# Performance work log

Hardware: AMD Instinct MI355X
Metric: run time of the kernel (lower is better)

Reference implementation:

```python
import jax, jax.numpy as jnp
import numpy as np

N_HEAD = 8
REG_LAMBDA = 0.01


def setup_inputs() -> dict:
    key = jax.random.key(0)
    k0, k1, k2 = jax.random.split(key, 3)
    B, T, C = 8, 256, 512
    x = jax.random.normal(k0, (B, T, C), dtype=jnp.float32)
    W_attn = jax.random.normal(k1, (3 * C, C), dtype=jnp.float32) * 0.02
    b_attn = jnp.zeros((3 * C,), dtype=jnp.float32)
    W_proj = jax.random.normal(k2, (C, C), dtype=jnp.float32) * 0.02
    b_proj = jnp.zeros((C,), dtype=jnp.float32)
    return {"x": x, "W_attn": W_attn, "b_attn": b_attn, "W_proj": W_proj, "b_proj": b_proj}


def reference(x, W_attn, b_attn, W_proj, b_proj):
    B, T, C = x.shape
    H = N_HEAD
    hs = C // H
    # qkv projection (nn.Linear: x @ W.T + b)
    qkv = x @ W_attn.T + b_attn                      # [B,T,3C]
    q, k, v = jnp.split(qkv, 3, axis=-1)

    def to_heads(t):
        return t.reshape(B, T, H, hs).transpose(0, 2, 1, 3)  # [B,H,T,hs]

    q, k, v = to_heads(q), to_heads(k), to_heads(v)

    scale = 1.0 / jnp.sqrt(jnp.asarray(hs, dtype=x.dtype))
    scores = jnp.einsum('bhqd,bhkd->bhqk', q, k) * scale     # [B,H,T,T]
    causal = jnp.tril(jnp.ones((T, T), dtype=bool))
    scores = jnp.where(causal, scores, -jnp.inf)
    att = jax.nn.softmax(scores, axis=-1)                    # [B,H,T,T]

    # --- Soft DPP penalty ---
    # For token i: G_i = (sqrt(w_i) outer sqrt(w_i)) * (K K^T) + 1e-6 I,
    # which equals (sqrt_w * K) @ (sqrt_w * K)^T from the original code.
    KKt = jnp.einsum('bhid,bhjd->bhij', k, k)                # [B,H,T,T], shared across tokens
    eyeT = 1e-6 * jnp.eye(T, dtype=jnp.float32)

    def step(carry, w):  # w: [B,H,T] attention row for one query token
        s = jnp.sqrt(w + 1e-8)                               # [B,H,T]
        G = (s[..., :, None] * s[..., None, :] * KKt).astype(jnp.float32) + eyeT
        det = jnp.linalg.det(G)                              # [B,H]
        return carry + jnp.sum(jnp.log(det + 1e-8)), None

    att_tok = jnp.moveaxis(att, 2, 0)                        # [T,B,H,T]
    logdet_sum, _ = jax.lax.scan(step, jnp.float32(0.0), att_tok)
    dpp_penalty = REG_LAMBDA * (-1.0 * logdet_sum)

    # attention output
    y = jnp.einsum('bhqk,bhkd->bhqd', att, v)                # [B,H,T,hs]
    y = y.transpose(0, 2, 1, 3).reshape(B, T, C)
    y = y @ W_proj.T + b_proj
    return y, dpp_penalty
```

## Files before the change

kernel.cpp:

```cpp
#include <hip/hip_runtime.h>
#include <hip/hip_bf16.h>
#include <math.h>


#define BT 2048
#define TSEQ 256
#define CDIM 512
#define QKVC 1536

typedef __attribute__((ext_vector_type(8))) short bf16x8;
typedef __attribute__((ext_vector_type(4))) float f32x4;

__device__ __forceinline__ unsigned short b16(float f) {
  return __builtin_bit_cast(unsigned short, __float2bfloat16(f));
}

__global__ __launch_bounds__(256) void qkv_mfma(
    const float* __restrict__ X, const float* __restrict__ W,
    const float* __restrict__ bias, unsigned short* __restrict__ C,
    unsigned short* __restrict__ VT) {
  __shared__ unsigned short a_s[64][68];
  __shared__ unsigned short b_s[64][68];

  const int t  = threadIdx.x;
  const int m0 = blockIdx.x * 64;
  const int n0 = blockIdx.y * 64;
  const int w  = t >> 6, l = t & 63;
  const int wm = (w >> 1) * 32, wn = (w & 1) * 32;

  f32x4 acc[2][2];
#pragma unroll
  for (int i = 0; i < 2; i++)
#pragma unroll
    for (int j = 0; j < 2; j++) acc[i][j] = (f32x4){0.f, 0.f, 0.f, 0.f};

  float4 pa[4], pb[4];
  auto prefetch = [&](int k0) {
#pragma unroll
    for (int u = 0; u < 4; u++) {
      const int id = t + u * 256;
      const int r  = id >> 4;
      const int c4 = (id & 15) << 2;
      pa[u] = *(const float4*)&X[(size_t)(m0 + r) * CDIM + k0 + c4];
      pb[u] = *(const float4*)&W[(size_t)(n0 + r) * CDIM + k0 + c4];
    }
  };

  prefetch(0);
  for (int kb = 0; kb < CDIM / 64; kb++) {
    __syncthreads();
#pragma unroll
    for (int u = 0; u < 4; u++) {
      const int id = t + u * 256;
      const int r  = id >> 4;
      const int c4 = (id & 15) << 2;
      ushort4 ah;
      ah.x = b16(pa[u].x); ah.y = b16(pa[u].y); ah.z = b16(pa[u].z); ah.w = b16(pa[u].w);
      *(ushort4*)&a_s[r][c4] = ah;
      ushort4 bh;
      bh.x = b16(pb[u].x); bh.y = b16(pb[u].y); bh.z = b16(pb[u].z); bh.w = b16(pb[u].w);
      *(ushort4*)&b_s[r][c4] = bh;
    }
    __syncthreads();
    if (kb + 1 < CDIM / 64) prefetch((kb + 1) * 64);

#pragma unroll
    for (int ks = 0; ks < 2; ks++) {
      const int fr = l & 15;
      const int fk = ks * 32 + ((l >> 4) << 3);
      bf16x8 fa[2], fb[2];
#pragma unroll
      for (int mt = 0; mt < 2; mt++) fa[mt] = *(const bf16x8*)&a_s[wm + mt * 16 + fr][fk];
#pragma unroll
      for (int nt = 0; nt < 2; nt++) fb[nt] = *(const bf16x8*)&b_s[wn + nt * 16 + fr][fk];
#pragma unroll
      for (int mt = 0; mt < 2; mt++)
#pragma unroll
        for (int nt = 0; nt < 2; nt++)
          acc[mt][nt] = __builtin_amdgcn_mfma_f32_16x16x32_bf16(fa[mt], fb[nt], acc[mt][nt], 0, 0, 0);
    }
  }

  const int cl = l & 15, rq = (l >> 4) << 2;
  if (n0 < 1024) {
    const float scale = (n0 < 512) ? 0.125f : 1.0f;
#pragma unroll
    for (int nt = 0; nt < 2; nt++) {
      const int col = n0 + wn + nt * 16 + cl;
      const float bv = bias[col];
#pragma unroll
      for (int mt = 0; mt < 2; mt++) {
        const int row = m0 + wm + mt * 16 + rq;
#pragma unroll
        for (int r = 0; r < 4; r++)
          C[(size_t)(row + r) * QKVC + col] = b16((acc[mt][nt][r] + bv) * scale);
      }
    }
  } else {
#pragma unroll
    for (int nt = 0; nt < 2; nt++) {
      const int col  = n0 + wn + nt * 16 + cl;
      const float bv = bias[col];
      const int hcol = col - 1024;
      const int h = hcol >> 6, d = hcol & 63;
#pragma unroll
      for (int mt = 0; mt < 2; mt++) {
        const int row = m0 + wm + mt * 16 + rq;
        const int b = row >> 8, j = row & 255;
        ushort4 o;
        o.x = b16(acc[mt][nt][0] + bv);
        o.y = b16(acc[mt][nt][1] + bv);
        o.z = b16(acc[mt][nt][2] + bv);
        o.w = b16(acc[mt][nt][3] + bv);
        *(ushort4*)&VT[(((size_t)(b * 8 + h) * 64 + d) << 8) + j] = o;
      }
    }
  }
}

__global__ __launch_bounds__(256) void attn_mfma(
    const unsigned short* __restrict__ qkv, const unsigned short* __restrict__ VT,
    unsigned short* __restrict__ y) {
  __shared__ unsigned short k_s[64][72];
  __shared__ unsigned short vt_s[64][72];
  __shared__ unsigned short q_s2[2][32][72];
  __shared__ unsigned short p_s[4][16][72];

  const int t  = threadIdx.x;
  const int qp = blockIdx.x;
  const int bh = blockIdx.y;
  const int b  = bh >> 3, h = bh & 7;
  const int w  = t >> 6, l = t & 63;
  const int half = w >> 1;
  const int ww   = w & 1;
  const int qt = qp * 2 + half;
  const int q0 = qt * 32;
  const size_t rowbase = (size_t)b * TSEQ * QKVC + h * 64;
  const size_t vtb = (size_t)bh << 14;
  const float NEG = -1e30f;

#pragma unroll
  for (int u = 0; u < 2; u++) {
    const int id = t + u * 256;
    const int rg = id >> 3, c8 = (id & 7) << 3;
    const int hf = rg >> 5, row = rg & 31;
    const int qrow = (qp * 2 + hf) * 32 + row;
    *(uint4*)&q_s2[hf][row][c8] =
        *(const uint4*)(qkv + rowbase + (size_t)qrow * QKVC + c8);
  }
  __syncthreads();

  const int m  = l & 15;
  const int q4 = l >> 4;
  const int ko = q4 << 3;

  bf16x8 qf[2];
#pragma unroll
  for (int kb = 0; kb < 2; kb++)
    qf[kb] = *(const bf16x8*)&q_s2[half][ww * 16 + m][kb * 32 + ko];

  f32x4 acc_y[4];
  float m_i[4], Zp[4];
#pragma unroll
  for (int r = 0; r < 4; r++) {
    acc_y[r] = (f32x4){0.f, 0.f, 0.f, 0.f};
    m_i[r] = NEG; Zp[r] = 0.f;
  }

  const int ntiles = qp + 1;

  uint4 pk[2], pv[2];
  auto loadKV = [&](int jt) {
#pragma unroll
    for (int u = 0; u < 2; u++) {
      const int id = t + u * 256;
      const int r = id >> 3, c8 = (id & 7) << 3;
      pk[u] = *(const uint4*)(qkv + rowbase + (size_t)(jt * 64 + r) * QKVC + 512 + c8);
      pv[u] = *(const uint4*)(VT + vtb + ((size_t)r << 8) + jt * 64 + c8);
    }
  };

  loadKV(0);
  for (int jt = 0; jt < ntiles; jt++) {
    __syncthreads();
#pragma unroll
    for (int u = 0; u < 2; u++) {
      const int id = t + u * 256;
      const int r = id >> 3, c8 = (id & 7) << 3;
      *(uint4*)&k_s[r][c8]  = pk[u];
      *(uint4*)&vt_s[r][c8] = pv[u];
    }
    __syncthreads();
    if (jt + 1 < ntiles) loadKV(jt + 1);

    f32x4 s[4];
#pragma unroll
    for (int nt = 0; nt < 4; nt++) s[nt] = (f32x4){0.f, 0.f, 0.f, 0.f};
#pragma unroll
    for (int nt = 0; nt < 4; nt++)
#pragma unroll
      for (int kb = 0; kb < 2; kb++) {
        const bf16x8 kf = *(const bf16x8*)&k_s[nt * 16 + m][kb * 32 + ko];
        s[nt] = __builtin_amdgcn_mfma_f32_16x16x32_bf16(qf[kb], kf, s[nt], 0, 0, 0);
      }

    const bool diag = (jt == ntiles - 1);
#pragma unroll
    for (int reg = 0; reg < 4; reg++) {
      const int i = q0 + ww * 16 + q4 * 4 + reg;
      float pvv[4];
      float vmax = NEG;
#pragma unroll
      for (int nt = 0; nt < 4; nt++) {
        float sv = s[nt][reg];
        if (diag && (jt * 64 + nt * 16 + m) > i) sv = NEG;
        pvv[nt] = sv;
        vmax = fmaxf(vmax, sv);
      }
      vmax = fmaxf(vmax, __shfl_xor(vmax, 1));
      vmax = fmaxf(vmax, __shfl_xor(vmax, 2));
      vmax = fmaxf(vmax, __shfl_xor(vmax, 4));
      vmax = fmaxf(vmax, __shfl_xor(vmax, 8));
      const float mnew  = fmaxf(m_i[reg], vmax);
      const float alpha = __expf(m_i[reg] - mnew);
      m_i[reg] = mnew;
      float zs = 0.f;
#pragma unroll
      for (int nt = 0; nt < 4; nt++) {
        const float p = __expf(pvv[nt] - mnew);
        p_s[w][q4 * 4 + reg][nt * 16 + m] = b16(p);
        zs += p;
      }
      Zp[reg] = Zp[reg] * alpha + zs;
#pragma unroll
      for (int nt2 = 0; nt2 < 4; nt2++) acc_y[nt2][reg] *= alpha;
    }
    __syncthreads();

#pragma unroll
    for (int kb2 = 0; kb2 < 2; kb2++) {
      const bf16x8 pf = *(const bf16x8*)&p_s[w][m][kb2 * 32 + ko];
#pragma unroll
      for (int nt2 = 0; nt2 < 4; nt2++) {
        const bf16x8 vf = *(const bf16x8*)&vt_s[nt2 * 16 + m][kb2 * 32 + ko];
        acc_y[nt2] = __builtin_amdgcn_mfma_f32_16x16x32_bf16(pf, vf, acc_y[nt2], 0, 0, 0);
      }
    }
  }

#pragma unroll
  for (int reg = 0; reg < 4; reg++) {
    float z = Zp[reg];
    z += __shfl_xor(z, 1);
    z += __shfl_xor(z, 2);
    z += __shfl_xor(z, 4);
    z += __shfl_xor(z, 8);
    const float inv = 1.0f / z;
    const int i = q0 + ww * 16 + q4 * 4 + reg;
#pragma unroll
    for (int nt2 = 0; nt2 < 4; nt2++)
      y[((size_t)(b * TSEQ + i)) * CDIM + h * 64 + nt2 * 16 + m] =
          b16(acc_y[nt2][reg] * inv);
  }
}

__global__ __launch_bounds__(256) void proj_mfma(
    const unsigned short* __restrict__ A, const float* __restrict__ B,
    const float* __restrict__ bias, float* __restrict__ C) {
  __shared__ unsigned short a_s[32][68];
  __shared__ unsigned short b_s[64][68];

  const int t  = threadIdx.x;
  if (blockIdx.x == 0 && blockIdx.y == 0 && t == 0) {
    const double log_1em8 = -18.420680743952367;
    C[(size_t)BT * CDIM] = (float)(-0.01 * (16384.0 * log_1em8));
  }
  const int m0 = blockIdx.x * 32;
  const int n0 = blockIdx.y * 64;
  const int w  = t >> 6, l = t & 63;
  const int wm = (w >> 1) * 16, wn = (w & 1) * 32;

  f32x4 acc[2];
#pragma unroll
  for (int j = 0; j < 2; j++) acc[j] = (f32x4){0.f, 0.f, 0.f, 0.f};

  uint4  pa;
  float4 pb[4];
  auto prefetch = [&](int k0) {
    {
      const int r = t >> 3, c8 = (t & 7) << 3;
      pa = *(const uint4*)(A + (size_t)(m0 + r) * CDIM + k0 + c8);
    }
#pragma unroll
    for (int u = 0; u < 4; u++) {
      const int id = t + u * 256;
      const int r = id >> 4, c4 = (id & 15) << 2;
      pb[u] = *(const float4*)&B[(size_t)(n0 + r) * CDIM + k0 + c4];
    }
  };

  prefetch(0);
  for (int kb = 0; kb < CDIM / 64; kb++) {
    __syncthreads();
    {
      const int r = t >> 3, c8 = (t & 7) << 3;
      *(uint4*)&a_s[r][c8] = pa;
    }
#pragma unroll
    for (int u = 0; u < 4; u++) {
      const int id = t + u * 256;
      const int r = id >> 4, c4 = (id & 15) << 2;
      ushort4 bh;
      bh.x = b16(pb[u].x); bh.y = b16(pb[u].y); bh.z = b16(pb[u].z); bh.w = b16(pb[u].w);
      *(ushort4*)&b_s[r][c4] = bh;
    }
    __syncthreads();
    if (kb + 1 < CDIM / 64) prefetch((kb + 1) * 64);

#pragma unroll
    for (int ks = 0; ks < 2; ks++) {
      const int fr = l & 15;
      const int fk = ks * 32 + ((l >> 4) << 3);
      const bf16x8 fa = *(const bf16x8*)&a_s[wm + fr][fk];
      bf16x8 fb2[2];
#pragma unroll
      for (int nt = 0; nt < 2; nt++) fb2[nt] = *(const bf16x8*)&b_s[wn + nt * 16 + fr][fk];
#pragma unroll
      for (int nt = 0; nt < 2; nt++)
        acc[nt] = __builtin_amdgcn_mfma_f32_16x16x32_bf16(fa, fb2[nt], acc[nt], 0, 0, 0);
    }
  }

  const int cl = l & 15, rq = (l >> 4) << 2;
#pragma unroll
  for (int nt = 0; nt < 2; nt++) {
    const int col = n0 + wn + nt * 16 + cl;
    const float bv = bias[col];
    const int row = m0 + wm + rq;
#pragma unroll
    for (int r = 0; r < 4; r++)
      C[(size_t)(row + r) * CDIM + col] = acc[nt][r] + bv;
  }
}

extern "C" void kernel_launch(void* const* d_in, const int* in_sizes, int n_in,
                              void* d_out, int out_size, void* d_ws, size_t ws_size,
                              hipStream_t stream) {
  const float* x      = (const float*)d_in[0];
  const float* W_attn = (const float*)d_in[1];
  const float* b_attn = (const float*)d_in[2];
  const float* W_proj = (const float*)d_in[3];
  const float* b_proj = (const float*)d_in[4];
  float* out = (float*)d_out;

  char* wsb = (char*)d_ws;
  unsigned short* qkv_bf = (unsigned short*)wsb;
  unsigned short* vt_bf  = (unsigned short*)(wsb + 6291456);
  unsigned short* y_bf   = (unsigned short*)(wsb + 8388608);

  qkv_mfma<<<dim3(32, 24), 256, 0, stream>>>(x, W_attn, b_attn, qkv_bf, vt_bf);

  attn_mfma<<<dim3(4, 64), 256, 0, stream>>>(qkv_bf, vt_bf, y_bf);

  proj_mfma<<<dim3(64, 8), 256, 0, stream>>>(y_bf, W_proj, b_proj, out);
}
```

Measured before the change: 98.56 us.

## Fuse output projection into attention kernel with atomic head accumulation

Removes the separate projection kernel. Each attention block converts its head's slice of W_proj to bf16 in shared memory, multiplies its 64-row y tile by it, and atomically adds the partial result into the fp32 output. The qkv kernel now pre-initializes the output with the projection bias and writes the penalty constant. This avoids the y round trip through memory and one launch, but adds 8-way float atomics per output element, large LDS use, heavy accumulator register pressure and redundant W_proj loads per block.

After: 120.5 us. 1.22x slower.

```diff
diff --git a/kernel.cpp b/kernel.cpp
--- a/kernel.cpp
+++ b/kernel.cpp
@@ -15,16 +15,36 @@
   return __builtin_bit_cast(unsigned short, __float2bfloat16(f));
 }
 
+__device__ __forceinline__ void atomAddF32(float* p, float v) {
+  unsafeAtomicAdd(p, v);
+}
+
 __global__ __launch_bounds__(256) void qkv_mfma(
     const float* __restrict__ X, const float* __restrict__ W,
     const float* __restrict__ bias, unsigned short* __restrict__ C,
-    unsigned short* __restrict__ VT) {
+    unsigned short* __restrict__ VT, const float* __restrict__ b_proj,
+    float* __restrict__ out) {
   __shared__ unsigned short a_s[64][68];
   __shared__ unsigned short b_s[64][68];
 
   const int t  = threadIdx.x;
   const int m0 = blockIdx.x * 64;
   const int n0 = blockIdx.y * 64;
+
+  if (blockIdx.y == 0) {
+#pragma unroll
+    for (int u = 0; u < 32; u++) {
+      const int id = t + u * 256;
+      const int r  = id >> 7;
+      const int c  = (id & 127) << 2;
+      *(float4*)&out[(size_t)(m0 + r) * CDIM + c] = *(const float4*)&b_proj[c];
+    }
+    if (blockIdx.x == 0 && t == 0) {
+      const double log_1em8 = -18.420680743952367;
+      out[(size_t)BT * CDIM] = (float)(-0.01 * (16384.0 * log_1em8));
+    }
+  }
+
   const int w  = t >> 6, l = t & 63;
   const int wm = (w >> 1) * 32, wn = (w & 1) * 32;
 
@@ -118,13 +138,15 @@
   }
 }
 
-__global__ __launch_bounds__(256) void attn_mfma(
+__global__ __launch_bounds__(256) void attn_proj(
     const unsigned short* __restrict__ qkv, const unsigned short* __restrict__ VT,
-    unsigned short* __restrict__ y) {
+    const float* __restrict__ Wp, float* __restrict__ out) {
   __shared__ unsigned short k_s[64][72];
   __shared__ unsigned short vt_s[64][72];
   __shared__ unsigned short q_s2[2][32][72];
   __shared__ unsigned short p_s[4][16][72];
+  __shared__ unsigned short y_s[64][72];
+  __shared__ unsigned short w_s[512][68];
 
   const int t  = threadIdx.x;
   const int qp = blockIdx.x;
@@ -256,90 +278,69 @@
     z += __shfl_xor(z, 4);
     z += __shfl_xor(z, 8);
     const float inv = 1.0f / z;
-    const int i = q0 + ww * 16 + q4 * 4 + reg;
+    const int lr = half * 32 + ww * 16 + q4 * 4 + reg;
 #pragma unroll
     for (int nt2 = 0; nt2 < 4; nt2++)
-      y[((size_t)(b * TSEQ + i)) * CDIM + h * 64 + nt2 * 16 + m] =
-          b16(acc_y[nt2][reg] * inv);
-  }
-}
-
-__global__ __launch_bounds__(256) void proj_mfma(
-    const unsigned short* __restrict__ A, const float* __restrict__ B,
-    const float* __restrict__ bias, float* __restrict__ C) {
-  __shared__ unsigned short a_s[32][68];
-  __shared__ unsigned short b_s[64][68];
-
-  const int t  = threadIdx.x;
-  if (blockIdx.x == 0 && blockIdx.y == 0 && t == 0) {
-    const double log_1em8 = -18.420680743952367;
-    C[(size_t)BT * CDIM] = (float)(-0.01 * (16384.0 * log_1em8));
-  }
-  const int m0 = blockIdx.x * 32;
-  const int n0 = blockIdx.y * 64;
-  const int w  = t >> 6, l = t & 63;
-  const int wm = (w >> 1) * 16, wn = (w & 1) * 32;
-
-  f32x4 acc[2];
-#pragma unroll
-  for (int j = 0; j < 2; j++) acc[j] = (f32x4){0.f, 0.f, 0.f, 0.f};
-
-  uint4  pa;
-  float4 pb[4];
-  auto prefetch = [&](int k0) {
-    {
-      const int r = t >> 3, c8 = (t & 7) << 3;
-      pa = *(const uint4*)(A + (size_t)(m0 + r) * CDIM + k0 + c8);
-    }
-#pragma unroll
-    for (int u = 0; u < 4; u++) {
-      const int id = t + u * 256;
-      const int r = id >> 4, c4 = (id & 15) << 2;
-      pb[u] = *(const float4*)&B[(size_t)(n0 + r) * CDIM + k0 + c4];
-    }
-  };
-
-  prefetch(0);
-  for (int kb = 0; kb < CDIM / 64; kb++) {
-    __syncthreads();
-    {
-      const int r = t >> 3, c8 = (t & 7) << 3;
-      *(uint4*)&a_s[r][c8] = pa;
-    }
-#pragma unroll
-    for (int u = 0; u < 4; u++) {
-      const int id = t + u * 256;
-      const int r = id >> 4, c4 = (id & 15) << 2;
-      ushort4 bh;
-      bh.x = b16(pb[u].x); bh.y = b16(pb[u].y); bh.z = b16(pb[u].z); bh.w = b16(pb[u].w);
-      *(ushort4*)&b_s[r][c4] = bh;
-    }
-    __syncthreads();
-    if (kb + 1 < CDIM / 64) prefetch((kb + 1) * 64);
+      y_s[lr][nt2 * 16 + m] = b16(acc_y[nt2][reg] * inv);
+  }
+
+  {
+    float4 wv[8];
+    for (int cu = 0; cu < 4; cu++) {
+#pragma unroll
+      for (int u = 0; u < 8; u++) {
+        const int id = (cu * 8 + u) * 256 + t;
+        const int r = id >> 4, c4 = (id & 15) << 2;
+        wv[u] = *(const float4*)&Wp[(size_t)r * CDIM + h * 64 + c4];
+      }
+#pragma unroll
+      for (int u = 0; u < 8; u++) {
+        const int id = (cu * 8 + u) * 256 + t;
+        const int r = id >> 4, c4 = (id & 15) << 2;
+        ushort4 o;
+        o.x = b16(wv[u].x); o.y = b16(wv[u].y); o.z = b16(wv[u].z); o.w = b16(wv[u].w);
+        *(ushort4*)&w_s[r][c4] = o;
+      }
+    }
+  }
+  __syncthreads();
+
+  {
+    const int fr = l & 15;
+    const int cl2 = l & 15, rq2 = (l >> 4) << 2;
+    f32x4 po[4][8];
+#pragma unroll
+    for (int i = 0; i < 4; i++)
+#pragma unroll
+      for (int j = 0; j < 8; j++) po[i][j] = (f32x4){0.f, 0.f, 0.f, 0.f};
 
 #pragma unroll
     for (int ks = 0; ks < 2; ks++) {
-      const int fr = l & 15;
       const int fk = ks * 32 + ((l >> 4) << 3);
-      const bf16x8 fa = *(const bf16x8*)&a_s[wm + fr][fk];
-      bf16x8 fb2[2];
-#pragma unroll
-      for (int nt = 0; nt < 2; nt++) fb2[nt] = *(const bf16x8*)&b_s[wn + nt * 16 + fr][fk];
-#pragma unroll
-      for (int nt = 0; nt < 2; nt++)
-        acc[nt] = __builtin_amdgcn_mfma_f32_16x16x32_bf16(fa, fb2[nt], acc[nt], 0, 0, 0);
-    }
-  }
-
-  const int cl = l & 15, rq = (l >> 4) << 2;
-#pragma unroll
-  for (int nt = 0; nt < 2; nt++) {
-    const int col = n0 + wn + nt * 16 + cl;
-    const float bv = bias[col];
-    const int row = m0 + wm + rq;
-#pragma unroll
-    for (int r = 0; r < 4; r++)
-      C[(size_t)(row + r) * CDIM + col] = acc[nt][r] + bv;
+      bf16x8 fa[4], fb[8];
+#pragma unroll
+      for (int mt = 0; mt < 4; mt++) fa[mt] = *(const bf16x8*)&y_s[mt * 16 + fr][fk];
+#pragma unroll
+      for (int nt = 0; nt < 8; nt++) fb[nt] = *(const bf16x8*)&w_s[w * 128 + nt * 16 + fr][fk];
+#pragma unroll
+      for (int mt = 0; mt < 4; mt++)
+#pragma unroll
+        for (int nt = 0; nt < 8; nt++)
+          po[mt][nt] = __builtin_amdgcn_mfma_f32_16x16x32_bf16(fa[mt], fb[nt], po[mt][nt], 0, 0, 0);
+    }
+
+    const size_t rowbase_out = (size_t)b * TSEQ + qp * 64;
+#pragma unroll
+    for (int nt = 0; nt < 8; nt++) {
+      const int col = w * 128 + nt * 16 + cl2;
+#pragma unroll
+      for (int mt = 0; mt < 4; mt++) {
+        const int row = mt * 16 + rq2;
+#pragma unroll
+        for (int r = 0; r < 4; r++)
+          atomAddF32(&out[(rowbase_out + row + r) * CDIM + col], po[mt][nt][r]);
+      }
+    }
   }
 }
 
@@ -356,11 +357,9 @@
   char* wsb = (char*)d_ws;
   unsigned short* qkv_bf = (unsigned short*)wsb;
   unsigned short* vt_bf  = (unsigned short*)(wsb + 6291456);
-  unsigned short* y_bf   = (unsigned short*)(wsb + 8388608);
-
-  qkv_mfma<<<dim3(32, 24), 256, 0, stream>>>(x, W_attn, b_attn, qkv_bf, vt_bf);
-
-  attn_mfma<<<dim3(4, 64), 256, 0, stream>>>(qkv_bf, vt_bf, y_bf);
-
-  proj_mfma<<<dim3(64, 8), 256, 0, stream>>>(y_bf, W_proj, b_proj, out);
-}
+
+  qkv_mfma<<<dim3(32, 24), 256, 0, stream>>>(x, W_attn, b_attn, qkv_bf, vt_bf,
+                                             b_proj, out);
+
+  attn_proj<<<dim3(4, 64), 256, 0, stream>>>(qkv_bf, vt_bf, W_proj, out);
+}
```
